# Optimization experiments

Hardware: AMD Instinct MI355X
Metric: run time of the kernel (lower is better)

## Reference

```python
import jax, jax.numpy as jnp
import numpy as np

INPUT_DIM = 256
NODE_DIM = 6
OUTPUT_DIM = 256
N_NODES = 10000
N_EDGES = 320000


def setup_inputs() -> dict:
    key = jax.random.key(0)
    ks = jax.random.split(key, 6)
    x = jax.random.normal(ks[0], (N_NODES, NODE_DIM), dtype=jnp.float32)
    edge_index = jax.random.randint(ks[1], (2, N_EDGES), 0, N_NODES, dtype=jnp.int64 if jax.config.jax_enable_x64 else jnp.int32)
    edge_attr = jax.random.normal(ks[2], (N_EDGES, INPUT_DIM), dtype=jnp.float32)
    mask = jax.random.uniform(ks[3], (N_EDGES,), dtype=jnp.float32)
    in_feat = INPUT_DIM * 3 + NODE_DIM * 2  # 774
    limit = float(np.sqrt(6.0 / (in_feat + OUTPUT_DIM)))  # xavier_uniform
    W = jax.random.uniform(ks[4], (OUTPUT_DIM, in_feat), dtype=jnp.float32, minval=-limit, maxval=limit)
    b = jax.random.uniform(ks[5], (OUTPUT_DIM,), dtype=jnp.float32, minval=-1.0 / np.sqrt(in_feat), maxval=1.0 / np.sqrt(in_feat))
    return {"x": x, "num_nodes": N_NODES, "edge_index": edge_index, "edge_attr": edge_attr, "mask": mask, "W": W, "b": b}


def reference(x, num_nodes, edge_index, edge_attr, mask, W, b):
    row = edge_index[0]
    col = edge_index[1]
    # masked mean-ish aggregation of edge features into destination nodes
    num = jax.ops.segment_sum(edge_attr * mask[:, None], col, num_segments=num_nodes)  # [N, input_dim]
    den = jax.ops.segment_sum(mask[:, None], col, num_segments=num_nodes)             # [N, 1]
    node_rep = num / (den + 1.0)
    node_rep = jnp.concatenate([node_rep, x], axis=1)  # [N, input_dim + node_dim]
    edge_rep = jnp.concatenate([node_rep[row], node_rep[col], edge_attr], axis=-1)  # [E, 3*input_dim + 2*node_dim]
    edge_rep = edge_rep @ W.T + b  # [E, output_dim]
    return (node_rep, edge_rep)
```

## Files before the change

kernel.cpp:

```cpp
#include <hip/hip_runtime.h>
#include <hip/hip_bf16.h>
#include <stdint.h>

typedef __attribute__((ext_vector_type(4))) float f32x4;
typedef __attribute__((ext_vector_type(8))) short bf16x8;

#define NDIM 6
#define IN_DIM 256
#define OUT_DIM 256
#define KW 780
#define NR 262
#define NRP 264
#define K2 832
#define BM 64
#define BK 64
#define NT 13
#define SCAN_T 1024

__device__ __forceinline__ short f2bf(float f) {
  return __builtin_bit_cast(short, __float2bfloat16(f));
}

__device__ __forceinline__ void gload_lds16(void* lds, const void* g) {
  __builtin_amdgcn_global_load_lds(
      (const __attribute__((address_space(1))) unsigned int*)g,
      (__attribute__((address_space(3))) unsigned int*)lds, 16, 0, 0);
}

__global__ void hist_kernel(const int* __restrict__ ei, int* __restrict__ counts, int E) {
  int e = blockIdx.x * 256 + threadIdx.x;
  if (e < E) atomicAdd(&counts[ei[(long)E + e]], 1);
}

__global__ __launch_bounds__(SCAN_T) void scan_kernel(const int* __restrict__ counts,
                                                      int* __restrict__ offsets, int N) {
  __shared__ int part[SCAN_T];
  int t = threadIdx.x;
  int chunk = (N + SCAN_T - 1) / SCAN_T;
  int begin = t * chunk;
  int s = 0;
  for (int i = 0; i < chunk; ++i) {
    int idx = begin + i;
    if (idx < N) s += counts[idx];
  }
  part[t] = s;
  __syncthreads();
  for (int d = 1; d < SCAN_T; d <<= 1) {
    int v = (t >= d) ? part[t - d] : 0;
    __syncthreads();
    part[t] += v;
    __syncthreads();
  }
  int run = (t == 0) ? 0 : part[t - 1];
  for (int i = 0; i < chunk; ++i) {
    int idx = begin + i;
    if (idx < N) { offsets[idx] = run; run += counts[idx]; }
  }
}

__global__ void scatter_kernel(const int* __restrict__ ei, const int* __restrict__ offsets,
                               int* __restrict__ cursor, int* __restrict__ csr, int E) {
  int e = blockIdx.x * 256 + threadIdx.x;
  if (e >= E) return;
  int col = ei[(long)E + e];
  int pos = atomicAdd(&cursor[col], 1);
  csr[offsets[col] + pos] = e;
}

__global__ __launch_bounds__(256) void reduce_kernel(
    const int* __restrict__ csr, const int* __restrict__ offsets,
    const int* __restrict__ counts, const float* __restrict__ ea,
    const float* __restrict__ mask, const float* __restrict__ x,
    float* __restrict__ outN, short* __restrict__ nrepb, int N) {
  int n = blockIdx.x * 4 + (threadIdx.x >> 6);
  if (n >= N) return;
  int lane = threadIdx.x & 63;
  int s = offsets[n], cnt = counts[n];
  f32x4 sum = (f32x4)0.0f;
  float den = 0.0f;
#pragma unroll 4
  for (int i = 0; i < cnt; ++i) {
    int e = csr[s + i];
    float m = mask[e];
    den += m;
    f32x4 v = ((const f32x4*)ea)[(long)e * 64 + lane];
    sum.x += v.x * m; sum.y += v.y * m; sum.z += v.z * m; sum.w += v.w * m;
  }
  float inv = 1.0f / (den + 1.0f);
  sum.x *= inv; sum.y *= inv; sum.z *= inv; sum.w *= inv;
  float* po = outN + (long)n * NR + lane * 4;
  po[0] = sum.x; po[1] = sum.y; po[2] = sum.z; po[3] = sum.w;
  short4 pb;
  pb.x = f2bf(sum.x); pb.y = f2bf(sum.y); pb.z = f2bf(sum.z); pb.w = f2bf(sum.w);
  *(short4*)(nrepb + (long)n * NRP + lane * 4) = pb;
  if (lane < NDIM) {
    float xv = x[(long)n * NDIM + lane];
    outN[(long)n * NR + IN_DIM + lane] = xv;
    nrepb[(long)n * NRP + IN_DIM + lane] = f2bf(xv);
  } else if (lane < 8) {
    nrepb[(long)n * NRP + IN_DIM + lane] = 0;
  }
}

__global__ void wprep_kernel(const float* __restrict__ W, short* __restrict__ Wtb) {
  int idx = blockIdx.x * 256 + threadIdx.x;
  if (idx >= OUT_DIM * K2) return;
  int n = idx / K2, k = idx % K2;
  float v = 0.0f;
  if (k < 256) {
    v = W[(long)n * KW + 524 + k];
  } else if (k < 520) {
    int kk = k - 256; if (kk < NR) v = W[(long)n * KW + kk];
  } else if (k < 784) {
    int kk = k - 520; if (kk < NR) v = W[(long)n * KW + NR + kk];
  }
  Wtb[idx] = f2bf(v);
}

__global__ __launch_bounds__(256, 2) void gemm_kernel(
    const int* __restrict__ ei, const float* __restrict__ ea,
    const short* __restrict__ nrepb, const short* __restrict__ Wtb,
    const float* __restrict__ bias, const short* __restrict__ zerobuf,
    float* __restrict__ outE, int E) {
  __shared__ short As[8][BM * BK];

  const int tid = threadIdx.x;
  const int wave = tid >> 6, lane = tid & 63;
  const long e0 = (long)blockIdx.x * BM;
  const int nbase = wave * 64;

  float bvals[4];
#pragma unroll
  for (int nf = 0; nf < 4; ++nf) bvals[nf] = bias[nbase + 16 * nf + (lane & 15)];

  const int scp = lane & 7;
  int srow[2], ridx[2], cidx[2];
  srow[0] = 16 * wave + (lane >> 3);
  srow[1] = srow[0] + 8;
#pragma unroll
  for (int i = 0; i < 2; ++i) {
    long ec = e0 + srow[i]; if (ec >= E) ec = E - 1;
    ridx[i] = ei[ec];
    cidx[i] = ei[(long)E + ec];
  }

  f32x4 acc[4][4];
#pragma unroll
  for (int mf = 0; mf < 4; ++mf)
#pragma unroll
    for (int nf = 0; nf < 4; ++nf) acc[mf][nf] = (f32x4)0.0f;

  bf16x8 bv[2][8];

  auto loadB = [&](int tt, int tb) {
#pragma unroll
    for (int s2 = 0; s2 < 2; ++s2)
#pragma unroll
      for (int nf = 0; nf < 4; ++nf)
        bv[tb][s2 * 4 + nf] = *(const bf16x8*)&Wtb[
            (long)(nbase + nf * 16 + (lane & 15)) * K2 + tt * BK + s2 * 32 + (lane >> 4) * 8];
  };

  auto stage_nr = [&](int t) {
#pragma unroll
    for (int i = 0; i < 2; ++i) {
      int row = srow[i];
      int c = scp ^ (row & 7);
      int k = t * BK + 8 * c;
      const short* src;
      if (k < 520)      src = nrepb + (long)ridx[i] * NRP + (k - 256);
      else if (k < 784) src = nrepb + (long)cidx[i] * NRP + (k - 520);
      else              src = zerobuf;
      gload_lds16(&As[(t & 3) + 4][(16 * wave + i * 8) * BK], src);
    }
  };

  auto compute = [&](int t, int slot) {
#pragma unroll
    for (int s2 = 0; s2 < 2; ++s2) {
      bf16x8 a[4];
      int cl = s2 * 4 + (lane >> 4);
#pragma unroll
      for (int mf = 0; mf < 4; ++mf) {
        int m = 16 * mf + (lane & 15);
        a[mf] = *(const bf16x8*)&As[slot][m * BK + ((cl ^ (m & 7)) * 8)];
      }
      __builtin_amdgcn_s_setprio(1);
#pragma unroll
      for (int mf = 0; mf < 4; ++mf)
#pragma unroll
        for (int nf = 0; nf < 4; ++nf)
          acc[mf][nf] = __builtin_amdgcn_mfma_f32_16x16x32_bf16(
              a[mf], bv[t & 1][s2 * 4 + nf], acc[mf][nf], 0, 0, 0);
      __builtin_amdgcn_s_setprio(0);
    }
  };

  f32x4 eh[4][2][2];
#pragma unroll
  for (int t = 0; t < 4; ++t)
#pragma unroll
    for (int i = 0; i < 2; ++i) {
      int g = tid + i * 256;
      int row = g >> 3, cp = g & 7;
      int c = cp ^ (row & 7);
      long e = e0 + row; if (e >= E) e = E - 1;
      const f32x4* s = (const f32x4*)(ea + (e * IN_DIM + t * BK + 8 * c));
      eh[t][i][0] = s[0];
      eh[t][i][1] = s[1];
    }
  loadB(0, 0);
  stage_nr(4);
  stage_nr(5);
  __builtin_amdgcn_sched_barrier(0);
#pragma unroll
  for (int t = 0; t < 4; ++t)
#pragma unroll
    for (int i = 0; i < 2; ++i) {
      int g = tid + i * 256;
      int row = g >> 3, cp = g & 7;
      f32x4 v0 = eh[t][i][0], v1 = eh[t][i][1];
      bf16x8 p;
      p[0] = f2bf(v0.x); p[1] = f2bf(v0.y); p[2] = f2bf(v0.z); p[3] = f2bf(v0.w);
      p[4] = f2bf(v1.x); p[5] = f2bf(v1.y); p[6] = f2bf(v1.z); p[7] = f2bf(v1.w);
      *(bf16x8*)&As[t][row * BK + cp * 8] = p;
    }
  asm volatile("s_waitcnt vmcnt(4) lgkmcnt(0)" ::: "memory");
  __builtin_amdgcn_s_barrier();
  __builtin_amdgcn_sched_barrier(0);

#pragma unroll
  for (int t = 0; t < NT; ++t) {
    if (t >= 4 && t <= 10) stage_nr(t + 2);
    if (t + 1 < NT) loadB(t + 1, (t + 1) & 1);
    if (t >= 1 && t <= 3)        asm volatile("s_waitcnt vmcnt(8)" ::: "memory");
    else if (t >= 4 && t <= 10)  asm volatile("s_waitcnt vmcnt(10)" ::: "memory");
    else if (t == 11)            asm volatile("s_waitcnt vmcnt(8)" ::: "memory");
    else if (t == 12)            asm volatile("s_waitcnt vmcnt(0)" ::: "memory");
    if (t < 12) {
      __builtin_amdgcn_s_barrier();
      __builtin_amdgcn_sched_barrier(0);
    }
    compute(t, t < 4 ? t : (t & 3) + 4);
  }

#pragma unroll
  for (int mf = 0; mf < 4; ++mf) {
#pragma unroll
    for (int nf = 0; nf < 4; ++nf) {
#pragma unroll
      for (int q = 0; q < 4; ++q) {
        long e = e0 + 16 * mf + (lane >> 4) * 4 + q;
        if (e < E)
          outE[e * OUT_DIM + nbase + 16 * nf + (lane & 15)] = acc[mf][nf][q] + bvals[nf];
      }
    }
  }
}

extern "C" void kernel_launch(void* const* d_in, const int* in_sizes, int n_in,
                              void* d_out, int out_size, void* d_ws, size_t ws_size,
                              hipStream_t stream) {
  const float* x    = (const float*)d_in[0];
  const int*   ei   = (const int*)d_in[2];
  const float* ea   = (const float*)d_in[3];
  const float* mask = (const float*)d_in[4];
  const float* W    = (const float*)d_in[5];
  const float* b    = (const float*)d_in[6];
  const int E = in_sizes[4];
  const int N = in_sizes[0] / NDIM;

  char* p = (char*)d_ws;
  int* counts  = (int*)p; p += (long)N * 4;
  int* cursor  = (int*)p; p += (long)N * 4;
  int* offsets = (int*)p; p += (long)(N + 1) * 4;
  int* csr     = (int*)p; p += (long)E * 4;
  p = (char*)(((uintptr_t)p + 15) & ~(uintptr_t)15);
  float* zerobuf = (float*)p; p += 64 * 4;
  short* nrepb   = (short*)p; p += (long)N * NRP * 2;
  short* Wtb     = (short*)p;

  float* outN = (float*)d_out;
  float* outE = outN + (long)N * NR;

  hipMemsetAsync(counts, 0, (size_t)2 * N * 4, stream);
  hipMemsetAsync(zerobuf, 0, 64 * 4, stream);

  hist_kernel<<<(E + 255) / 256, 256, 0, stream>>>(ei, counts, E);
  scan_kernel<<<1, SCAN_T, 0, stream>>>(counts, offsets, N);
  scatter_kernel<<<(E + 255) / 256, 256, 0, stream>>>(ei, offsets, cursor, csr, E);
  reduce_kernel<<<(N + 3) / 4, 256, 0, stream>>>(csr, offsets, counts, ea, mask, x,
                                                 outN, nrepb, N);
  wprep_kernel<<<(OUT_DIM * K2 + 255) / 256, 256, 0, stream>>>(W, Wtb);
  gemm_kernel<<<(E + BM - 1) / BM, 256, 0, stream>>>(ei, ea, nrepb, Wtb, b,
                                                     (const short*)zerobuf, outE, E);
}
```

Before: 462.5 us.

## Precompute per-node projections and shrink the edge GEMM to edge_attr only

The edge linear layer is split into two parts. A new node-level GEMM computes node_rep@W_row^T + b and node_rep@W_col^T for all N nodes into fp32 tables Pr and Pc. The per-edge GEMM then only multiplies edge_attr (K=256) and gathers-adds Pr[row] + Pc[col] in the epilogue. This replaces the K=832 per-edge GEMM and its per-edge bf16 node-row gathers with a much smaller GEMM plus two fp32 1KB row gathers per edge. The nrepb stride becomes 320 with padding columns 264–319 never initialised. Those columns rely on zero weights, so garbage in uninitialised workspace (for example NaN bits) could leak into the results.

After: 392.0 us. 15.2% less time.

```diff
diff --git a/kernel.cpp b/kernel.cpp
--- a/kernel.cpp
+++ b/kernel.cpp
@@ -10,11 +10,7 @@
 #define OUT_DIM 256
 #define KW 780
 #define NR 262
-#define NRP 264
-#define K2 832
-#define BM 64
-#define BK 64
-#define NT 13
+#define NRP 320
 #define SCAN_T 1024
 
 __device__ __forceinline__ short f2bf(float f) {
@@ -102,80 +98,81 @@
   }
 }
 
-__global__ void wprep_kernel(const float* __restrict__ W, short* __restrict__ Wtb) {
+__global__ void wprep_kernel(const float* __restrict__ W, short* __restrict__ Weat,
+                             short* __restrict__ Wrt, short* __restrict__ Wct) {
   int idx = blockIdx.x * 256 + threadIdx.x;
-  if (idx >= OUT_DIM * K2) return;
-  int n = idx / K2, k = idx % K2;
-  float v = 0.0f;
-  if (k < 256) {
-    v = W[(long)n * KW + 524 + k];
-  } else if (k < 520) {
-    int kk = k - 256; if (kk < NR) v = W[(long)n * KW + kk];
-  } else if (k < 784) {
-    int kk = k - 520; if (kk < NR) v = W[(long)n * KW + NR + kk];
-  }
-  Wtb[idx] = f2bf(v);
-}
-
-__global__ __launch_bounds__(256, 2) void gemm_kernel(
-    const int* __restrict__ ei, const float* __restrict__ ea,
-    const short* __restrict__ nrepb, const short* __restrict__ Wtb,
-    const float* __restrict__ bias, const short* __restrict__ zerobuf,
-    float* __restrict__ outE, int E) {
-  __shared__ short As[8][BM * BK];
-
+  if (idx < OUT_DIM * 256) {
+    int n = idx >> 8, k = idx & 255;
+    Weat[idx] = f2bf(W[(long)n * KW + 2 * NR + k]);
+    return;
+  }
+  idx -= OUT_DIM * 256;
+  if (idx < OUT_DIM * NRP) {
+    int n = idx / NRP, k = idx % NRP;
+    Wrt[idx] = f2bf(k < NR ? W[(long)n * KW + k] : 0.0f);
+    return;
+  }
+  idx -= OUT_DIM * NRP;
+  if (idx < OUT_DIM * NRP) {
+    int n = idx / NRP, k = idx % NRP;
+    Wct[idx] = f2bf(k < NR ? W[(long)n * KW + NR + k] : 0.0f);
+  }
+}
+
+__global__ __launch_bounds__(256, 2) void pgemm_kernel(
+    const short* __restrict__ nrepb, const short* __restrict__ Wrt,
+    const short* __restrict__ Wct, const float* __restrict__ bias,
+    float* __restrict__ Pr, float* __restrict__ Pc, int N) {
+  __shared__ short As[5][64 * 64];
   const int tid = threadIdx.x;
   const int wave = tid >> 6, lane = tid & 63;
-  const long e0 = (long)blockIdx.x * BM;
+  const int m0 = blockIdx.x * 64;
+  const int table = blockIdx.y;
+  const short* Wt = table ? Wct : Wrt;
+  float* P = table ? Pc : Pr;
   const int nbase = wave * 64;
 
   float bvals[4];
 #pragma unroll
-  for (int nf = 0; nf < 4; ++nf) bvals[nf] = bias[nbase + 16 * nf + (lane & 15)];
+  for (int nf = 0; nf < 4; ++nf)
+    bvals[nf] = table ? 0.0f : bias[nbase + 16 * nf + (lane & 15)];
+
+  f32x4 acc[4][4];
+#pragma unroll
+  for (int mf = 0; mf < 4; ++mf)
+#pragma unroll
+    for (int nf = 0; nf < 4; ++nf) acc[mf][nf] = (f32x4)0.0f;
+
+  bf16x8 bv[2][8];
+  auto loadB = [&](int t, int tb) {
+#pragma unroll
+    for (int s2 = 0; s2 < 2; ++s2)
+#pragma unroll
+      for (int nf = 0; nf < 4; ++nf)
+        bv[tb][s2 * 4 + nf] = *(const bf16x8*)&Wt[
+            (long)(nbase + nf * 16 + (lane & 15)) * NRP + t * 64 + s2 * 32 + (lane >> 4) * 8];
+  };
 
   const int scp = lane & 7;
-  int srow[2], ridx[2], cidx[2];
-  srow[0] = 16 * wave + (lane >> 3);
-  srow[1] = srow[0] + 8;
-#pragma unroll
-  for (int i = 0; i < 2; ++i) {
-    long ec = e0 + srow[i]; if (ec >= E) ec = E - 1;
-    ridx[i] = ei[ec];
-    cidx[i] = ei[(long)E + ec];
-  }
-
-  f32x4 acc[4][4];
-#pragma unroll
-  for (int mf = 0; mf < 4; ++mf)
-#pragma unroll
-    for (int nf = 0; nf < 4; ++nf) acc[mf][nf] = (f32x4)0.0f;
-
-  bf16x8 bv[2][8];
-
-  auto loadB = [&](int tt, int tb) {
-#pragma unroll
-    for (int s2 = 0; s2 < 2; ++s2)
-#pragma unroll
-      for (int nf = 0; nf < 4; ++nf)
-        bv[tb][s2 * 4 + nf] = *(const bf16x8*)&Wtb[
-            (long)(nbase + nf * 16 + (lane & 15)) * K2 + tt * BK + s2 * 32 + (lane >> 4) * 8];
-  };
-
-  auto stage_nr = [&](int t) {
+#pragma unroll
+  for (int t = 0; t < 5; ++t)
 #pragma unroll
     for (int i = 0; i < 2; ++i) {
-      int row = srow[i];
+      int row = 16 * wave + 8 * i + (lane >> 3);
       int c = scp ^ (row & 7);
-      int k = t * BK + 8 * c;
-      const short* src;
-      if (k < 520)      src = nrepb + (long)ridx[i] * NRP + (k - 256);
-      else if (k < 784) src = nrepb + (long)cidx[i] * NRP + (k - 520);
-      else              src = zerobuf;
-      gload_lds16(&As[(t & 3) + 4][(16 * wave + i * 8) * BK], src);
+      long m = m0 + row; if (m >= N) m = N - 1;
+      gload_lds16(&As[t][(16 * wave + 8 * i) * 64], nrepb + m * NRP + t * 64 + 8 * c);
     }
-  };
-
-  auto compute = [&](int t, int slot) {
+  loadB(0, 0);
+  asm volatile("s_waitcnt vmcnt(8)" ::: "memory");
+  __builtin_amdgcn_s_barrier();
+  __builtin_amdgcn_sched_barrier(0);
+
+#pragma unroll
+  for (int t = 0; t < 5; ++t) {
+    if (t < 4) loadB(t + 1, (t + 1) & 1);
+    if (t < 4) asm volatile("s_waitcnt vmcnt(8)" ::: "memory");
+    else       asm volatile("s_waitcnt vmcnt(0)" ::: "memory");
 #pragma unroll
     for (int s2 = 0; s2 < 2; ++s2) {
       bf16x8 a[4];
@@ -183,76 +180,121 @@
 #pragma unroll
       for (int mf = 0; mf < 4; ++mf) {
         int m = 16 * mf + (lane & 15);
-        a[mf] = *(const bf16x8*)&As[slot][m * BK + ((cl ^ (m & 7)) * 8)];
+        a[mf] = *(const bf16x8*)&As[t][m * 64 + ((cl ^ (m & 7)) * 8)];
       }
-      __builtin_amdgcn_s_setprio(1);
 #pragma unroll
       for (int mf = 0; mf < 4; ++mf)
 #pragma unroll
         for (int nf = 0; nf < 4; ++nf)
           acc[mf][nf] = __builtin_amdgcn_mfma_f32_16x16x32_bf16(
               a[mf], bv[t & 1][s2 * 4 + nf], acc[mf][nf], 0, 0, 0);
-      __builtin_amdgcn_s_setprio(0);
     }
+  }
+
+#pragma unroll
+  for (int mf = 0; mf < 4; ++mf)
+#pragma unroll
+    for (int nf = 0; nf < 4; ++nf)
+#pragma unroll
+      for (int q = 0; q < 4; ++q) {
+        long m = m0 + 16 * mf + (lane >> 4) * 4 + q;
+        if (m < N)
+          P[m * OUT_DIM + nbase + 16 * nf + (lane & 15)] = acc[mf][nf][q] + bvals[nf];
+      }
+}
+
+__global__ __launch_bounds__(256, 2) void egemm_kernel(
+    const int* __restrict__ ei, const float* __restrict__ ea,
+    const short* __restrict__ Weat, const float* __restrict__ Pr,
+    const float* __restrict__ Pc, float* __restrict__ outE, int E) {
+  __shared__ short As[4][64 * 64];
+  const int tid = threadIdx.x;
+  const int wave = tid >> 6, lane = tid & 63;
+  const long e0 = (long)blockIdx.x * 64;
+  const int nbase = wave * 64;
+
+  f32x4 acc[4][4];
+#pragma unroll
+  for (int mf = 0; mf < 4; ++mf)
+#pragma unroll
+    for (int nf = 0; nf < 4; ++nf) acc[mf][nf] = (f32x4)0.0f;
+
+  bf16x8 bv[2][8];
+  auto loadB = [&](int t, int tb) {
+#pragma unroll
+    for (int s2 = 0; s2 < 2; ++s2)
+#pragma unroll
+      for (int nf = 0; nf < 4; ++nf)
+        bv[tb][s2 * 4 + nf] = *(const bf16x8*)&Weat[
+            (nbase + nf * 16 + (lane & 15)) * 256 + t * 64 + s2 * 32 + (lane >> 4) * 8];
   };
 
-  f32x4 eh[4][2][2];
-#pragma unroll
-  for (int t = 0; t < 4; ++t)
-#pragma unroll
-    for (int i = 0; i < 2; ++i) {
-      int g = tid + i * 256;
-      int row = g >> 3, cp = g & 7;
-      int c = cp ^ (row & 7);
-      long e = e0 + row; if (e >= E) e = E - 1;
-      const f32x4* s = (const f32x4*)(ea + (e * IN_DIM + t * BK + 8 * c));
-      eh[t][i][0] = s[0];
-      eh[t][i][1] = s[1];
-    }
+  f32x4 eh[8][2];
+#pragma unroll
+  for (int j = 0; j < 8; ++j) {
+    int c8 = tid + j * 256;
+    int row = c8 >> 5, cp8 = c8 & 31;
+    long e = e0 + row; if (e >= E) e = E - 1;
+    const f32x4* s = (const f32x4*)(ea + (e * IN_DIM + cp8 * 8));
+    eh[j][0] = s[0];
+    eh[j][1] = s[1];
+  }
   loadB(0, 0);
-  stage_nr(4);
-  stage_nr(5);
   __builtin_amdgcn_sched_barrier(0);
 #pragma unroll
-  for (int t = 0; t < 4; ++t)
-#pragma unroll
-    for (int i = 0; i < 2; ++i) {
-      int g = tid + i * 256;
-      int row = g >> 3, cp = g & 7;
-      f32x4 v0 = eh[t][i][0], v1 = eh[t][i][1];
-      bf16x8 p;
-      p[0] = f2bf(v0.x); p[1] = f2bf(v0.y); p[2] = f2bf(v0.z); p[3] = f2bf(v0.w);
-      p[4] = f2bf(v1.x); p[5] = f2bf(v1.y); p[6] = f2bf(v1.z); p[7] = f2bf(v1.w);
-      *(bf16x8*)&As[t][row * BK + cp * 8] = p;
-    }
-  asm volatile("s_waitcnt vmcnt(4) lgkmcnt(0)" ::: "memory");
+  for (int j = 0; j < 8; ++j) {
+    int c8 = tid + j * 256;
+    int row = c8 >> 5, cp8 = c8 & 31;
+    int t = cp8 >> 3, cp = cp8 & 7;
+    f32x4 v0 = eh[j][0], v1 = eh[j][1];
+    bf16x8 p;
+    p[0] = f2bf(v0.x); p[1] = f2bf(v0.y); p[2] = f2bf(v0.z); p[3] = f2bf(v0.w);
+    p[4] = f2bf(v1.x); p[5] = f2bf(v1.y); p[6] = f2bf(v1.z); p[7] = f2bf(v1.w);
+    *(bf16x8*)&As[t][row * 64 + ((cp ^ (row & 7)) * 8)] = p;
+  }
+  asm volatile("s_waitcnt lgkmcnt(0)" ::: "memory");
   __builtin_amdgcn_s_barrier();
   __builtin_amdgcn_sched_barrier(0);
 
 #pragma unroll
-  for (int t = 0; t < NT; ++t) {
-    if (t >= 4 && t <= 10) stage_nr(t + 2);
-    if (t + 1 < NT) loadB(t + 1, (t + 1) & 1);
-    if (t >= 1 && t <= 3)        asm volatile("s_waitcnt vmcnt(8)" ::: "memory");
-    else if (t >= 4 && t <= 10)  asm volatile("s_waitcnt vmcnt(10)" ::: "memory");
-    else if (t == 11)            asm volatile("s_waitcnt vmcnt(8)" ::: "memory");
-    else if (t == 12)            asm volatile("s_waitcnt vmcnt(0)" ::: "memory");
-    if (t < 12) {
-      __builtin_amdgcn_s_barrier();
-      __builtin_amdgcn_sched_barrier(0);
+  for (int t = 0; t < 4; ++t) {
+    if (t < 3) loadB(t + 1, (t + 1) & 1);
+    if (t < 3) asm volatile("s_waitcnt vmcnt(8)" ::: "memory");
+    else       asm volatile("s_waitcnt vmcnt(0)" ::: "memory");
+#pragma unroll
+    for (int s2 = 0; s2 < 2; ++s2) {
+      bf16x8 a[4];
+      int cl = s2 * 4 + (lane >> 4);
+#pragma unroll
+      for (int mf = 0; mf < 4; ++mf) {
+        int m = 16 * mf + (lane & 15);
+        a[mf] = *(const bf16x8*)&As[t][m * 64 + ((cl ^ (m & 7)) * 8)];
+      }
+#pragma unroll
+      for (int mf = 0; mf < 4; ++mf)
+#pragma unroll
+        for (int nf = 0; nf < 4; ++nf)
+          acc[mf][nf] = __builtin_amdgcn_mfma_f32_16x16x32_bf16(
+              a[mf], bv[t & 1][s2 * 4 + nf], acc[mf][nf], 0, 0, 0);
     }
-    compute(t, t < 4 ? t : (t & 3) + 4);
   }
 
 #pragma unroll
   for (int mf = 0; mf < 4; ++mf) {
 #pragma unroll
-    for (int nf = 0; nf < 4; ++nf) {
-#pragma unroll
-      for (int q = 0; q < 4; ++q) {
-        long e = e0 + 16 * mf + (lane >> 4) * 4 + q;
-        if (e < E)
-          outE[e * OUT_DIM + nbase + 16 * nf + (lane & 15)] = acc[mf][nf][q] + bvals[nf];
+    for (int q = 0; q < 4; ++q) {
+      long e = e0 + 16 * mf + (lane >> 4) * 4 + q;
+      bool ok = e < E;
+      long ec = ok ? e : (E - 1);
+      int re = ei[ec], ce = ei[(long)E + ec];
+      const float* pr = Pr + (long)re * OUT_DIM;
+      const float* pc = Pc + (long)ce * OUT_DIM;
+      if (ok) {
+#pragma unroll
+        for (int nf = 0; nf < 4; ++nf) {
+          int n = nbase + 16 * nf + (lane & 15);
+          outE[e * OUT_DIM + n] = acc[mf][nf][q] + pr[n] + pc[n];
+        }
       }
     }
   }
@@ -276,22 +318,26 @@
   int* offsets = (int*)p; p += (long)(N + 1) * 4;
   int* csr     = (int*)p; p += (long)E * 4;
   p = (char*)(((uintptr_t)p + 15) & ~(uintptr_t)15);
-  float* zerobuf = (float*)p; p += 64 * 4;
-  short* nrepb   = (short*)p; p += (long)N * NRP * 2;
-  short* Wtb     = (short*)p;
+  short* nrepb = (short*)p; p += (long)N * NRP * 2;
+  short* Weat  = (short*)p; p += (long)OUT_DIM * 256 * 2;
+  short* Wrt   = (short*)p; p += (long)OUT_DIM * NRP * 2;
+  short* Wct   = (short*)p; p += (long)OUT_DIM * NRP * 2;
+  float* Pr    = (float*)p; p += (long)N * OUT_DIM * 4;
+  float* Pc    = (float*)p;
 
   float* outN = (float*)d_out;
   float* outE = outN + (long)N * NR;
 
   hipMemsetAsync(counts, 0, (size_t)2 * N * 4, stream);
-  hipMemsetAsync(zerobuf, 0, 64 * 4, stream);
 
   hist_kernel<<<(E + 255) / 256, 256, 0, stream>>>(ei, counts, E);
   scan_kernel<<<1, SCAN_T, 0, stream>>>(counts, offsets, N);
   scatter_kernel<<<(E + 255) / 256, 256, 0, stream>>>(ei, offsets, cursor, csr, E);
   reduce_kernel<<<(N + 3) / 4, 256, 0, stream>>>(csr, offsets, counts, ea, mask, x,
                                                  outN, nrepb, N);
-  wprep_kernel<<<(OUT_DIM * K2 + 255) / 256, 256, 0, stream>>>(W, Wtb);
-  gemm_kernel<<<(E + BM - 1) / BM, 256, 0, stream>>>(ei, ea, nrepb, Wtb, b,
-                                                     (const short*)zerobuf, outE, E);
-}
+  int wtot = OUT_DIM * 256 + 2 * OUT_DIM * NRP;
+  wprep_kernel<<<(wtot + 255) / 256, 256, 0, stream>>>(W, Weat, Wrt, Wct);
+  dim3 pg((N + 63) / 64, 2);
+  pgemm_kernel<<<pg, 256, 0, stream>>>(nrepb, Wrt, Wct, b, Pr, Pc, N);
+  egemm_kernel<<<(E + 63) / 64, 256, 0, stream>>>(ei, ea, Weat, Pr, Pc, outE, E);
+}
```
